# Kernel optimization log

Hardware: AMD Instinct MI355X
Metric: run time of the kernel (lower is better)

## Reference

```python
import jax, jax.numpy as jnp
import numpy as np

M, N, K, D_IN = 200, 6, 25, 784
GAMMA, EPS = 0.5, 0.5
TOTAL = M * N


def setup_inputs() -> dict:
    key = jax.random.key(0)
    ks = jax.random.split(key, 8)
    B = 16384
    def lin(kk, shape, fan_in):
        bound = 1.0 / np.sqrt(fan_in)
        return jax.random.uniform(kk, shape, jnp.float32, -bound, bound)
    return {
        "batch_x": jax.random.normal(ks[0], (B, D_IN), jnp.float32),
        "Wa": lin(ks[1], (M, D_IN), D_IN),
        "ba": lin(ks[2], (M,), D_IN),
        "Wb": lin(ks[3], (TOTAL, TOTAL), TOTAL),
        "bb": lin(ks[4], (TOTAL,), TOTAL),
        "Wd": lin(ks[5], (D_IN, M), M),
        "bd": lin(ks[6], (D_IN,), M),
    }


def _step(params, carry, x):
    Wa, ba, Wb, bb, Wd, bd = params
    x_b, phi, psi = carry
    # sigma: per-group drive broadcast over cells + full recurrent term, shape (m, n)
    z_a = (Wa @ x + ba)[:, None]                      # (m, 1)
    z_b = (Wb @ x_b + bb).reshape(M, N)               # (m, n)
    sigma = z_a + z_b
    # inhibited activity
    pi = (1.0 - phi) * (sigma - sigma.min() + 1.0)    # (m, n)
    lambda_i = pi.max(axis=1)                         # (m,)
    # top-1 cell per group (scatter of topk indices == one-hot argmax)
    M_pi = jax.nn.one_hot(jnp.argmax(pi, axis=1), N, dtype=sigma.dtype)
    # top-k groups
    _, idx = jax.lax.top_k(lambda_i, K)
    M_lambda = jnp.zeros((M,), sigma.dtype).at[idx].set(1.0)[:, None]
    y = jnp.tanh(M_pi * M_lambda * sigma)             # (m, n)
    x_a_pred = Wd @ y.max(axis=1) + bd                # (D_in,)
    # memory / inhibition updates
    psi_n = jnp.maximum(EPS * psi, y)
    phi_n = jnp.maximum(GAMMA * phi, y)
    alpha = psi_n.sum()
    alpha = jnp.where(alpha == 0.0, 1.0, alpha)
    x_b_n = (psi_n / alpha).reshape(-1)
    # original detaches the recurrent state each step
    carry_n = (jax.lax.stop_gradient(x_b_n),
               jax.lax.stop_gradient(phi_n),
               jax.lax.stop_gradient(psi_n))
    return carry_n, x_a_pred


def reference(batch_x, Wa, ba, Wb, bb, Wd, bd):
    params = (Wa, ba, Wb, bb, Wd, bd)
    carry0 = (jnp.zeros((TOTAL,), batch_x.dtype),
              jnp.zeros((M, N), batch_x.dtype),
              jnp.zeros((M, N), batch_x.dtype))
    (x_b, phi, psi), preds = jax.lax.scan(
        lambda c, x: _step(params, c, x), carry0, batch_x)
    return preds, x_b, phi, psi
```

## Files before the change

### kernel.cpp

```cpp
#include <hip/hip_runtime.h>
#include <math.h>

#define Tn   16384
#define Mg   200
#define Nc   6
#define TOT  1200
#define Kk   25
#define Din  784

__global__ void transpose_k(const float* __restrict__ src, float* __restrict__ dst,
                            int R, int C) {
    __shared__ float tile[32][33];
    int bx = blockIdx.x * 32, by = blockIdx.y * 32;
    int x = bx + threadIdx.x;
    for (int j = 0; j < 32; j += 8) {
        int y = by + threadIdx.y + j;
        if (x < C && y < R) tile[threadIdx.y + j][threadIdx.x] = src[(size_t)y * C + x];
    }
    __syncthreads();
    int x2 = by + threadIdx.x;
    for (int j = 0; j < 32; j += 8) {
        int y2 = bx + threadIdx.y + j;
        if (x2 < R && y2 < C) dst[(size_t)y2 * R + x2] = tile[threadIdx.x][threadIdx.y + j];
    }
}

__global__ void za_k(const float* __restrict__ X, const float* __restrict__ Wa,
                     const float* __restrict__ ba, float* __restrict__ Za) {
    __shared__ float xs[16][788];
    const int tid = threadIdx.x;
    const int t0  = blockIdx.x * 16;
    for (int idx = tid; idx < 16 * Din; idx += 256) {
        int tt = idx / Din, kk = idx - tt * Din;
        xs[tt][kk] = X[(size_t)(t0 + tt) * Din + kk];
    }
    __syncthreads();
    const int tq = tid & 15, gq = tid >> 4;
    const float4* xrow = reinterpret_cast<const float4*>(&xs[tq][0]);
    for (int g = gq; g < Mg; g += 16) {
        float acc = ba[g];
        const float4* wrow = reinterpret_cast<const float4*>(Wa + (size_t)g * Din);
        for (int k4 = 0; k4 < Din / 4; ++k4) {
            float4 a = xrow[k4], b = wrow[k4];
            acc = fmaf(a.x, b.x, acc); acc = fmaf(a.y, b.y, acc);
            acc = fmaf(a.z, b.z, acc); acc = fmaf(a.w, b.w, acc);
        }
        Za[(size_t)(t0 + tq) * Mg + g] = acc;
    }
}

__launch_bounds__(256, 1)
__global__ void serial_k(const float* __restrict__ Za, const float* __restrict__ WbT,
                         const float* __restrict__ bb,
                         float* __restrict__ Yval, int* __restrict__ Yidx,
                         float* __restrict__ outTail) {
    __shared__ alignas(16) unsigned long long lamk[Mg];
    __shared__ alignas(16) float red[4];
    __shared__ float sel_d[Kk];
    __shared__ int   sel_o[Kk];

    const int tid = threadIdx.x;
    const bool own = (tid < Mg);
    const int b = Nc * tid;

    float u0=0.f,u1=0.f,u2=0.f,u3=0.f,u4=0.f,u5=0.f;
    float p0=0.f,p1=0.f,p2=0.f,p3=0.f,p4=0.f,p5=0.f;
    float b0=0.f,b1=0.f,b2=0.f,b3=0.f,b4=0.f,b5=0.f;
    float alpha = 0.f;
    float zb = 0.f;
    if (own) {
        b0=bb[b]; b1=bb[b+1]; b2=bb[b+2]; b3=bb[b+3]; b4=bb[b+4]; b5=bb[b+5];
        zb = Za[tid];
    }

    for (int t = 0; t < Tn; ++t) {
        float inv = (alpha == 0.f) ? 1.f : (1.f / alpha);
        float s0=0,s1=0,s2=0,s3=0,s4=0,s5=0;
        float lmin = INFINITY;
        if (own) {
            float c = zb;
            s0 = fmaf(u0, inv, b0 + c); s1 = fmaf(u1, inv, b1 + c);
            s2 = fmaf(u2, inv, b2 + c); s3 = fmaf(u3, inv, b3 + c);
            s4 = fmaf(u4, inv, b4 + c); s5 = fmaf(u5, inv, b5 + c);
            lmin = fminf(fminf(fminf(s0,s1),fminf(s2,s3)),fminf(s4,s5));
        }
        for (int o = 32; o; o >>= 1) lmin = fminf(lmin, __shfl_down(lmin, o));
        if ((tid & 63) == 0) red[tid >> 6] = lmin;
        __syncthreads();

        float zn = 0.f;
        if (own && t + 1 < Tn) zn = Za[(size_t)(t + 1) * Mg + tid];

        unsigned long long myk = 0ull;
        float sb = 0.f, pb = 0.f;
        int bj = 0;
        if (own) {
            float4 r4 = *reinterpret_cast<const float4*>(red);
            float m1 = 1.f - fminf(fminf(r4.x, r4.y), fminf(r4.z, r4.w));
            float best = -INFINITY;
            float sa[6] = {s0,s1,s2,s3,s4,s5};
            float pa[6] = {p0,p1,p2,p3,p4,p5};
            #pragma unroll
            for (int j = 0; j < Nc; ++j) {
                float pv = (1.f - pa[j]) * (sa[j] + m1);
                if (pv > best) { best = pv; bj = j; sb = sa[j]; pb = pa[j]; }
            }
            unsigned int ub = __float_as_uint(best);
            ub ^= (unsigned int)(((int)ub) >> 31) | 0x80000000u;
            myk = ((unsigned long long)ub << 32) | (unsigned long long)(0xFFFFFFFFu - (unsigned)tid);
            lamk[tid] = myk;
        }
        __syncthreads();

        float d = 0.f;
        if (own) {
            int r = 0;
            const ulonglong2* L = reinterpret_cast<const ulonglong2*>(lamk);
            #pragma unroll
            for (int q = 0; q < Mg / 2; ++q) {
                ulonglong2 kv = L[q];
                r += (kv.x > myk) + (kv.y > myk);
            }
            if (r < Kk) {
                float y = tanhf(sb);
                d = y - 0.5f * pb;
                d = (d > 0.f) ? d : 0.f;
                sel_d[r] = d;
                sel_o[r] = (b + bj) * TOT;
                Yval[(size_t)t * Kk + r] = fmaxf(y, 0.f);
                Yidx[(size_t)t * Kk + r] = tid;
            }
            p0 = 0.5f*p0 + ((bj==0)?d:0.f); p1 = 0.5f*p1 + ((bj==1)?d:0.f);
            p2 = 0.5f*p2 + ((bj==2)?d:0.f); p3 = 0.5f*p3 + ((bj==3)?d:0.f);
            p4 = 0.5f*p4 + ((bj==4)?d:0.f); p5 = 0.5f*p5 + ((bj==5)?d:0.f);
        }
        __syncthreads();

        if (own) {
            float sd_[Kk]; int so_[Kk];
            #pragma unroll
            for (int k = 0; k < Kk; ++k) { sd_[k] = sel_d[k]; so_[k] = sel_o[k]; }
            float asum = 0.f;
            #pragma unroll
            for (int k = 0; k < Kk; ++k) asum += sd_[k];
            alpha = 0.5f * alpha + asum;

            float a0=0.5f*u0, a1=0.5f*u1, a2=0.5f*u2, a3=0.5f*u3, a4=0.5f*u4, a5=0.5f*u5;
            #pragma unroll
            for (int k = 0; k < Kk; ++k) {
                const float* c = WbT + so_[k] + b;
                float2 x0 = *reinterpret_cast<const float2*>(c);
                float2 x1 = *reinterpret_cast<const float2*>(c + 2);
                float2 x2 = *reinterpret_cast<const float2*>(c + 4);
                float dk = sd_[k];
                a0 = fmaf(dk, x0.x, a0); a1 = fmaf(dk, x0.y, a1);
                a2 = fmaf(dk, x1.x, a2); a3 = fmaf(dk, x1.y, a3);
                a4 = fmaf(dk, x2.x, a4); a5 = fmaf(dk, x2.y, a5);
            }
            u0=a0; u1=a1; u2=a2; u3=a3; u4=a4; u5=a5;
            zb = zn;
        }
    }

    if (own) {
        float inv = (alpha == 0.f) ? 1.f : (1.f / alpha);
        float pa[6] = {p0,p1,p2,p3,p4,p5};
        #pragma unroll
        for (int j = 0; j < Nc; ++j) {
            outTail[b + j]           = pa[j] * inv;
            outTail[TOT + b + j]     = pa[j];
            outTail[2 * TOT + b + j] = pa[j];
        }
    }
}

__global__ void preds_k(const float* __restrict__ Yval, const int* __restrict__ Yidx,
                        const float* __restrict__ WdT, const float* __restrict__ bd,
                        float* __restrict__ out) {
    const int t = blockIdx.x;
    __shared__ float sv[Kk];
    __shared__ int   si[Kk];
    if (threadIdx.x < Kk) {
        sv[threadIdx.x] = Yval[(size_t)t * Kk + threadIdx.x];
        si[threadIdx.x] = Yidx[(size_t)t * Kk + threadIdx.x];
    }
    __syncthreads();
    for (int d = threadIdx.x; d < Din; d += 256) {
        float acc = bd[d];
        #pragma unroll
        for (int k = 0; k < Kk; ++k)
            acc = fmaf(sv[k], WdT[(size_t)si[k] * Din + d], acc);
        out[(size_t)t * Din + d] = acc;
    }
}

extern "C" void kernel_launch(void* const* d_in, const int* in_sizes, int n_in,
                              void* d_out, int out_size, void* d_ws, size_t ws_size,
                              hipStream_t stream) {
    const float* X  = (const float*)d_in[0];
    const float* Wa = (const float*)d_in[1];
    const float* ba = (const float*)d_in[2];
    const float* Wb = (const float*)d_in[3];
    const float* bb = (const float*)d_in[4];
    const float* Wd = (const float*)d_in[5];
    const float* bd = (const float*)d_in[6];
    float* out = (float*)d_out;

    float* w    = (float*)d_ws;
    float* Za   = w;
    float* WbT  = Za  + (size_t)Tn * Mg;
    float* WdT  = WbT + (size_t)TOT * TOT;
    float* Yv   = WdT + (size_t)Mg * Din;
    int*   Yi   = (int*)(Yv + (size_t)Tn * Kk);

    dim3 tb(32, 8);
    transpose_k<<<dim3((TOT + 31) / 32, (TOT + 31) / 32), tb, 0, stream>>>(Wb, WbT, TOT, TOT);
    transpose_k<<<dim3((Mg + 31) / 32, (Din + 31) / 32), tb, 0, stream>>>(Wd, WdT, Din, Mg);
    za_k<<<Tn / 16, 256, 0, stream>>>(X, Wa, ba, Za);
    serial_k<<<1, 256, 0, stream>>>(Za, WbT, bb, Yv, Yi, out + (size_t)Tn * Din);
    preds_k<<<Tn, 256, 0, stream>>>(Yv, Yi, WdT, bd, out);
}
```

Baseline: 78.03 ms.

## Pad transposed recurrent weights per group and batch selected-column loads

Wb is transposed into a layout where each group's 6 cells are padded to 8 floats, so each thread fetches its weights with one float4 plus one float2 load instead of three float2 loads. All 25 selected-column loads are issued before the FMA loop to expose memory-level parallelism in the serial kernel. The selected delta and column offset are packed into one 64-bit shared entry, and tanh is computed before the rank count so it overlaps. The cost is a larger workspace for the padded matrix and more registers for the batched loads.

```diff
diff --git a/kernel.cpp b/kernel.cpp
--- a/kernel.cpp
+++ b/kernel.cpp
@@ -7,6 +7,8 @@
 #define TOT  1200
 #define Kk   25
 #define Din  784
+#define PADG 8
+#define CST  (Mg * PADG)
 
 __global__ void transpose_k(const float* __restrict__ src, float* __restrict__ dst,
                             int R, int C) {
@@ -22,6 +24,23 @@
     for (int j = 0; j < 32; j += 8) {
         int y2 = bx + threadIdx.y + j;
         if (x2 < R && y2 < C) dst[(size_t)y2 * R + x2] = tile[threadIdx.x][threadIdx.y + j];
+    }
+}
+
+__global__ void wbT_pad_k(const float* __restrict__ Wb, float* __restrict__ WbTp) {
+    __shared__ float tile[32][33];
+    int e0 = blockIdx.x * 32, i0 = blockIdx.y * 32;
+    for (int j = 0; j < 32; j += 8) {
+        int i = i0 + threadIdx.y + j, e = e0 + threadIdx.x;
+        if (i < TOT && e < TOT) tile[threadIdx.y + j][threadIdx.x] = Wb[(size_t)i * TOT + e];
+    }
+    __syncthreads();
+    for (int j = 0; j < 32; j += 8) {
+        int e = e0 + threadIdx.y + j, i = i0 + threadIdx.x;
+        if (i < TOT && e < TOT) {
+            int g = i / 6, c = i - 6 * g;
+            WbTp[(size_t)e * CST + PADG * g + c] = tile[threadIdx.x][threadIdx.y + j];
+        }
     }
 }
 
@@ -50,14 +69,13 @@
 }
 
 __launch_bounds__(256, 1)
-__global__ void serial_k(const float* __restrict__ Za, const float* __restrict__ WbT,
+__global__ void serial_k(const float* __restrict__ Za, const float* __restrict__ WbTp,
                          const float* __restrict__ bb,
                          float* __restrict__ Yval, int* __restrict__ Yidx,
                          float* __restrict__ outTail) {
     __shared__ alignas(16) unsigned long long lamk[Mg];
+    __shared__ alignas(16) unsigned long long sel[26];
     __shared__ alignas(16) float red[4];
-    __shared__ float sel_d[Kk];
-    __shared__ int   sel_o[Kk];
 
     const int tid = threadIdx.x;
     const bool own = (tid < Mg);
@@ -72,6 +90,10 @@
         b0=bb[b]; b1=bb[b+1]; b2=bb[b+2]; b3=bb[b+3]; b4=bb[b+4]; b5=bb[b+5];
         zb = Za[tid];
     }
+    if (tid == 255) sel[25] = 0ull;
+    __syncthreads();
+
+    const float* basep = WbTp + PADG * tid;
 
     for (int t = 0; t < Tn; ++t) {
         float inv = (alpha == 0.f) ? 1.f : (1.f / alpha);
@@ -114,6 +136,9 @@
 
         float d = 0.f;
         if (own) {
+            float y  = tanhf(sb);
+            float yv = fmaxf(y, 0.f);
+            float dc = fmaxf(y - 0.5f * pb, 0.f);
             int r = 0;
             const ulonglong2* L = reinterpret_cast<const ulonglong2*>(lamk);
             #pragma unroll
@@ -122,12 +147,11 @@
                 r += (kv.x > myk) + (kv.y > myk);
             }
             if (r < Kk) {
-                float y = tanhf(sb);
-                d = y - 0.5f * pb;
-                d = (d > 0.f) ? d : 0.f;
-                sel_d[r] = d;
-                sel_o[r] = (b + bj) * TOT;
-                Yval[(size_t)t * Kk + r] = fmaxf(y, 0.f);
+                d = dc;
+                unsigned off = (unsigned)((b + bj) * CST);
+                sel[r] = ((unsigned long long)off << 32) |
+                         (unsigned long long)__float_as_uint(d);
+                Yval[(size_t)t * Kk + r] = yv;
                 Yidx[(size_t)t * Kk + r] = tid;
             }
             p0 = 0.5f*p0 + ((bj==0)?d:0.f); p1 = 0.5f*p1 + ((bj==1)?d:0.f);
@@ -137,25 +161,36 @@
         __syncthreads();
 
         if (own) {
-            float sd_[Kk]; int so_[Kk];
-            #pragma unroll
-            for (int k = 0; k < Kk; ++k) { sd_[k] = sel_d[k]; so_[k] = sel_o[k]; }
+            ulonglong2 sraw[13];
+            const ulonglong2* S = reinterpret_cast<const ulonglong2*>(sel);
+            #pragma unroll
+            for (int q = 0; q < 13; ++q) sraw[q] = S[q];
+            float sd[Kk]; int so[Kk];
+            #pragma unroll
+            for (int k = 0; k < Kk; ++k) {
+                unsigned long long v = (k & 1) ? sraw[k >> 1].y : sraw[k >> 1].x;
+                sd[k] = __uint_as_float((unsigned)v);
+                so[k] = (int)(v >> 32);
+            }
             float asum = 0.f;
             #pragma unroll
-            for (int k = 0; k < Kk; ++k) asum += sd_[k];
+            for (int k = 0; k < Kk; ++k) asum += sd[k];
             alpha = 0.5f * alpha + asum;
 
+            float4 va[Kk]; float2 vb[Kk];
+            #pragma unroll
+            for (int k = 0; k < Kk; ++k) {
+                const float* c = basep + so[k];
+                va[k] = *reinterpret_cast<const float4*>(c);
+                vb[k] = *reinterpret_cast<const float2*>(c + 4);
+            }
             float a0=0.5f*u0, a1=0.5f*u1, a2=0.5f*u2, a3=0.5f*u3, a4=0.5f*u4, a5=0.5f*u5;
             #pragma unroll
             for (int k = 0; k < Kk; ++k) {
-                const float* c = WbT + so_[k] + b;
-                float2 x0 = *reinterpret_cast<const float2*>(c);
-                float2 x1 = *reinterpret_cast<const float2*>(c + 2);
-                float2 x2 = *reinterpret_cast<const float2*>(c + 4);
-                float dk = sd_[k];
-                a0 = fmaf(dk, x0.x, a0); a1 = fmaf(dk, x0.y, a1);
-                a2 = fmaf(dk, x1.x, a2); a3 = fmaf(dk, x1.y, a3);
-                a4 = fmaf(dk, x2.x, a4); a5 = fmaf(dk, x2.y, a5);
+                float dk = sd[k];
+                a0 = fmaf(dk, va[k].x, a0); a1 = fmaf(dk, va[k].y, a1);
+                a2 = fmaf(dk, va[k].z, a2); a3 = fmaf(dk, va[k].w, a3);
+                a4 = fmaf(dk, vb[k].x, a4); a5 = fmaf(dk, vb[k].y, a5);
             }
             u0=a0; u1=a1; u2=a2; u3=a3; u4=a4; u5=a5;
             zb = zn;
@@ -208,15 +243,15 @@
 
     float* w    = (float*)d_ws;
     float* Za   = w;
-    float* WbT  = Za  + (size_t)Tn * Mg;
-    float* WdT  = WbT + (size_t)TOT * TOT;
-    float* Yv   = WdT + (size_t)Mg * Din;
+    float* WbTp = Za   + (size_t)Tn * Mg;
+    float* WdT  = WbTp + (size_t)TOT * CST;
+    float* Yv   = WdT  + (size_t)Mg * Din;
     int*   Yi   = (int*)(Yv + (size_t)Tn * Kk);
 
     dim3 tb(32, 8);
-    transpose_k<<<dim3((TOT + 31) / 32, (TOT + 31) / 32), tb, 0, stream>>>(Wb, WbT, TOT, TOT);
+    wbT_pad_k<<<dim3(38, 38), tb, 0, stream>>>(Wb, WbTp);
     transpose_k<<<dim3((Mg + 31) / 32, (Din + 31) / 32), tb, 0, stream>>>(Wd, WdT, Din, Mg);
     za_k<<<Tn / 16, 256, 0, stream>>>(X, Wa, ba, Za);
-    serial_k<<<1, 256, 0, stream>>>(Za, WbT, bb, Yv, Yi, out + (size_t)Tn * Din);
+    serial_k<<<1, 256, 0, stream>>>(Za, WbTp, bb, Yv, Yi, out + (size_t)Tn * Din);
     preds_k<<<Tn, 256, 0, stream>>>(Yv, Yi, WdT, bd, out);
 }
```

Result: slower. 82.81 ms (+6.1%).
